# Performance work log

Measured on AMD Instinct MI355X. Metric: run time of the kernel, lower is better.

The kernel has to match this reference:

```python
import jax, jax.numpy as jnp
import numpy as np


def setup_inputs() -> dict:
    key = jax.random.key(0)
    k1, k2 = jax.random.split(key)
    B, D = 4096, 128
    z1 = jax.random.normal(k1, (B, D), dtype=jnp.float32)
    z2 = jax.random.normal(k2, (B, D), dtype=jnp.float32)
    return {"z1": z1, "z2": z2}


def reference(z1, z2):
    # Faithful translation of _arccos_hessian from ArccosHessianCalculator.
    # z1, z2: [B, D]; returns stacked (H_11, H_12, H_22), each [B, D, D].
    B, D = z1.shape
    z1_norm = jnp.sqrt(jnp.sum(z1 * z1, axis=1))          # [B]
    z2_norm = jnp.sqrt(jnp.sum(z2 * z2, axis=1))          # [B]
    z1u = z1 / z1_norm[:, None]                            # z1_normalized [B, D]
    z2u = z2 / z2_norm[:, None]                            # z2_normalized [B, D]
    cos = jnp.sum(z1u * z2u, axis=1)                       # cosine [B]
    c = cos[:, None, None]                                 # broadcastable cosine
    eye = jnp.eye(D, dtype=z1.dtype)[None, :, :]           # identity, broadcast over B

    outer_11 = jnp.einsum("bi,bj->bij", z1u, z1u)
    outer_12 = jnp.einsum("bi,bj->bij", z1u, z2u)
    outer_21 = jnp.einsum("bi,bj->bij", z2u, z1u)
    outer_22 = jnp.einsum("bi,bj->bij", z2u, z2u)

    H_11 = c * eye + outer_12 + outer_21 - 3.0 * c * outer_11
    H_12 = -eye + outer_11 + outer_22 - c * outer_21
    H_22 = c * eye + outer_12 + outer_21 - 3.0 * c * outer_22

    inv11 = (1.0 / (z1_norm * z1_norm))[:, None, None]
    inv12 = (1.0 / (z1_norm * z2_norm))[:, None, None]
    inv22 = (1.0 / (z2_norm * z2_norm))[:, None, None]

    return jnp.stack([H_11 * inv11, H_12 * inv12, H_22 * inv22], axis=0)  # [3, B, D, D]
```

## Files before the change

kernel.cpp:

```cpp
#include <hip/hip_runtime.h>

#define D 128
#define BD (D * D)

typedef float v4f __attribute__((ext_vector_type(4)));

__global__ __launch_bounds__(256) void arccos_hess_kernel(
    const float* __restrict__ z1, const float* __restrict__ z2,
    float* __restrict__ out, int B) {
    const int b = blockIdx.x;
    const int t = threadIdx.x;

    __shared__ float u1[D], u2[D];
    __shared__ float ws1[4], ws2[4], ws12[4];

    float v1 = 0.f, v2 = 0.f;
    if (t < D) {
        v1 = z1[(size_t)b * D + t];
        v2 = z2[(size_t)b * D + t];
    }
    float s1 = v1 * v1, s2 = v2 * v2, s12 = v1 * v2;
#pragma unroll
    for (int off = 32; off > 0; off >>= 1) {
        s1  += __shfl_down(s1, off, 64);
        s2  += __shfl_down(s2, off, 64);
        s12 += __shfl_down(s12, off, 64);
    }
    const int wave = t >> 6, lane = t & 63;
    if (lane == 0) { ws1[wave] = s1; ws2[wave] = s2; ws12[wave] = s12; }
    __syncthreads();

    const float n1sq = ws1[0] + ws1[1] + ws1[2] + ws1[3];
    const float n2sq = ws2[0] + ws2[1] + ws2[2] + ws2[3];
    const float dot  = ws12[0] + ws12[1] + ws12[2] + ws12[3];
    const float n1 = sqrtf(n1sq), n2 = sqrtf(n2sq);
    const float inv11 = 1.0f / n1sq;
    const float inv22 = 1.0f / n2sq;
    const float inv12 = 1.0f / (n1 * n2);
    const float c  = dot * inv12;
    const float c3 = 3.0f * c;

    if (t < D) {
        u1[t] = v1 / n1;
        u2[t] = v2 / n2;
    }
    __syncthreads();

    const int j0 = (t & 31) << 2;
    const float uj1[4] = { u1[j0], u1[j0 + 1], u1[j0 + 2], u1[j0 + 3] };
    const float uj2[4] = { u2[j0], u2[j0 + 1], u2[j0 + 2], u2[j0 + 3] };

    float* out0 = out + (size_t)b * BD;
    float* out1 = out0 + (size_t)B * BD;
    float* out2 = out1 + (size_t)B * BD;

#pragma unroll
    for (int k = 0; k < 16; ++k) {
        const int i = (t >> 5) + (k << 3);
        const float a1 = u1[i];
        const float a2 = u2[i];

        v4f h11, h12, h22;
#pragma unroll
        for (int q = 0; q < 4; ++q) {
            const float b1 = uj1[q], b2 = uj2[q];
            const float o11 = a1 * b1;
            const float o12 = a1 * b2;
            const float o21 = a2 * b1;
            const float o22 = a2 * b2;
            const float s1221 = o12 + o21;
            const float diag = (i == j0 + q) ? 1.0f : 0.0f;
            h11[q] = (s1221 - c3 * o11 + c * diag) * inv11;
            h12[q] = (o11 + o22 - c * o21 - diag) * inv12;
            h22[q] = (s1221 - c3 * o22 + c * diag) * inv22;
        }
        const size_t off = (size_t)i * D + j0;
        *(v4f*)(out0 + off) = h11;
        *(v4f*)(out1 + off) = h12;
        *(v4f*)(out2 + off) = h22;
    }
}

extern "C" void kernel_launch(void* const* d_in, const int* in_sizes, int n_in,
                              void* d_out, int out_size, void* d_ws, size_t ws_size,
                              hipStream_t stream) {
    const float* z1 = (const float*)d_in[0];
    const float* z2 = (const float*)d_in[1];
    float* out = (float*)d_out;
    const int B = in_sizes[0] / D;
    arccos_hess_kernel<<<B, 256, 0, stream>>>(z1, z2, out, B);
}
```

Baseline: 786.1 us.

## Split into prep and flat grid-stride sweep kernel for contiguous stores

Adds a prep kernel that computes the normalized vectors and the per-row scalars (cosine and inverse norms) into workspace. A second kernel with a fixed 2048x256 grid then walks the whole 3xBxDxD output as one flat float4 index space, so each iteration's stores are fully contiguous across the grid instead of three strided output planes per block. This targets the write-bandwidth-bound output store pattern. In exchange it adds a second launch, reloads u and the scalars from global/cache on every iteration, and is hardcoded to B=4096 with a fallback to the old kernel.

```diff
diff --git a/kernel.cpp b/kernel.cpp
--- a/kernel.cpp
+++ b/kernel.cpp
@@ -4,6 +4,106 @@
 #define BD (D * D)
 
 typedef float v4f __attribute__((ext_vector_type(4)));
+
+__global__ __launch_bounds__(128) void prep_kernel(
+    const float* __restrict__ z1, const float* __restrict__ z2,
+    float* __restrict__ u1n, float* __restrict__ u2n,
+    float* __restrict__ scal) {
+    const int b = blockIdx.x;
+    const int t = threadIdx.x;
+
+    const float v1 = z1[(size_t)b * D + t];
+    const float v2 = z2[(size_t)b * D + t];
+    float s1 = v1 * v1, s2 = v2 * v2, s12 = v1 * v2;
+#pragma unroll
+    for (int off = 32; off > 0; off >>= 1) {
+        s1  += __shfl_down(s1, off, 64);
+        s2  += __shfl_down(s2, off, 64);
+        s12 += __shfl_down(s12, off, 64);
+    }
+    __shared__ float w1[2], w2[2], w12[2];
+    const int wave = t >> 6, lane = t & 63;
+    if (lane == 0) { w1[wave] = s1; w2[wave] = s2; w12[wave] = s12; }
+    __syncthreads();
+
+    const float n1sq = w1[0] + w1[1];
+    const float n2sq = w2[0] + w2[1];
+    const float dot  = w12[0] + w12[1];
+    const float n1 = sqrtf(n1sq), n2 = sqrtf(n2sq);
+
+    u1n[(size_t)b * D + t] = v1 / n1;
+    u2n[(size_t)b * D + t] = v2 / n2;
+    if (t == 0) {
+        const float inv12 = 1.0f / (n1 * n2);
+        v4f s;
+        s[0] = dot * inv12;
+        s[1] = 1.0f / n1sq;
+        s[2] = inv12;
+        s[3] = 1.0f / n2sq;
+        *(v4f*)(scal + b * 4) = s;
+    }
+}
+
+__global__ __launch_bounds__(256) void sweep_kernel(
+    const float* __restrict__ u1n, const float* __restrict__ u2n,
+    const float* __restrict__ scal, float* __restrict__ out) {
+    const unsigned tid = blockIdx.x * 256u + threadIdx.x;
+    v4f* o = (v4f*)out;
+
+#pragma unroll 2
+    for (int it = 0; it < 96; ++it) {
+        const unsigned s  = tid + (unsigned)it * 524288u;
+        const unsigned p  = s >> 24;
+        const unsigned r  = s & 0xFFFFFFu;
+        const unsigned b  = r >> 12;
+        const unsigned e  = r & 0xFFFu;
+        const unsigned i  = e >> 5;
+        const unsigned j0 = (e & 31u) << 2;
+
+        const float* u1b = u1n + ((size_t)b << 7);
+        const float* u2b = u2n + ((size_t)b << 7);
+        const float a1 = u1b[i];
+        const float a2 = u2b[i];
+        const v4f bj1 = *(const v4f*)(u1b + j0);
+        const v4f bj2 = *(const v4f*)(u2b + j0);
+        const v4f sc  = *(const v4f*)(scal + (b << 2));
+        const float c = sc[0];
+
+        v4f h;
+        if (p == 0) {
+            const float m = sc[1], c3 = 3.0f * c;
+#pragma unroll
+            for (int q = 0; q < 4; ++q) {
+                const float o11 = a1 * bj1[q];
+                const float o12 = a1 * bj2[q];
+                const float o21 = a2 * bj1[q];
+                const float dg  = (j0 + q == i) ? c : 0.0f;
+                h[q] = (o12 + o21 - c3 * o11 + dg) * m;
+            }
+        } else if (p == 1) {
+            const float m = sc[2];
+#pragma unroll
+            for (int q = 0; q < 4; ++q) {
+                const float o11 = a1 * bj1[q];
+                const float o21 = a2 * bj1[q];
+                const float o22 = a2 * bj2[q];
+                const float dg  = (j0 + q == i) ? 1.0f : 0.0f;
+                h[q] = (o11 + o22 - c * o21 - dg) * m;
+            }
+        } else {
+            const float m = sc[3], c3 = 3.0f * c;
+#pragma unroll
+            for (int q = 0; q < 4; ++q) {
+                const float o12 = a1 * bj2[q];
+                const float o21 = a2 * bj1[q];
+                const float o22 = a2 * bj2[q];
+                const float dg  = (j0 + q == i) ? c : 0.0f;
+                h[q] = (o12 + o21 - c3 * o22 + dg) * m;
+            }
+        }
+        o[s] = h;
+    }
+}
 
 __global__ __launch_bounds__(256) void arccos_hess_kernel(
     const float* __restrict__ z1, const float* __restrict__ z2,
@@ -88,5 +188,15 @@
     const float* z2 = (const float*)d_in[1];
     float* out = (float*)d_out;
     const int B = in_sizes[0] / D;
-    arccos_hess_kernel<<<B, 256, 0, stream>>>(z1, z2, out, B);
-}
+
+    const size_t need = (size_t)2 * 4096 * 128 * 4 + 4096 * 4 * 4;
+    if (B == 4096 && ws_size >= need) {
+        float* u1n  = (float*)d_ws;
+        float* u2n  = u1n + (size_t)4096 * 128;
+        float* scal = u2n + (size_t)4096 * 128;
+        prep_kernel<<<4096, 128, 0, stream>>>(z1, z2, u1n, u2n, scal);
+        sweep_kernel<<<2048, 256, 0, stream>>>(u1n, u2n, scal, out);
+    } else {
+        arccos_hess_kernel<<<B, 256, 0, stream>>>(z1, z2, out, B);
+    }
+}
```

Result: slower. 815.2 us (+3.7%).
